# Kernel tuning notes

Hardware: AMD Instinct MI355X
Metric: run time of the kernel (lower is better)

## Reference

```python
import jax, jax.numpy as jnp
import numpy as np


def setup_inputs() -> dict:
    key = jax.random.key(0)
    x = jax.random.normal(key, (32, 512, 56, 56), dtype=jnp.float32)
    return {"x": x}


def reference(x):
    n, c, h, w = x.shape
    f = x.reshape(n, c, h * w)                       # (n, c, hw)
    f_norm = jax.nn.softmax(f * 7.0, axis=2)         # softmax over spatial
    bilinear = jnp.einsum('ncs,nds->ncd', f_norm, f) # (n, c, c)
    bilinear = jax.nn.softmax(bilinear, axis=2)      # softmax over channel 'keys'
    trilinear = jnp.einsum('ncd,nds->ncs', bilinear, f).reshape(n, c, h, w)
    trilinear = jax.lax.stop_gradient(trilinear)     # matches torch .detach()
    structure_att = jnp.sum(trilinear, axis=1, keepdims=True)  # (n, 1, h, w)
    return structure_att
```

## Files before the change

kernel.cpp:

```cpp
#include <hip/hip_runtime.h>
#include <stdint.h>


#define NB 32
#define CC 512
#define SS 3136
#define SCALE 7.0f
#define K7F 10.098865286222744f
#define INVK7F 0.09902102579427789f

typedef float f32x4 __attribute__((ext_vector_type(4)));
typedef _Float16 f16x8 __attribute__((ext_vector_type(8)));
typedef _Float16 f16x4 __attribute__((ext_vector_type(4)));
typedef _Float16 f16x2 __attribute__((ext_vector_type(2)));

__device__ inline unsigned short f2bf(float f) {
  unsigned int u = __float_as_uint(f);
  u += 0x7fffu + ((u >> 16) & 1u);
  return (unsigned short)(u >> 16);
}
__device__ inline float bf2f(unsigned short u) {
  return __uint_as_float((uint32_t)u << 16);
}

__device__ inline float fast_exp2(float v) {
  float r;
  asm("v_exp_f32 %0, %1" : "=v"(r) : "v"(v));
  return r;
}
__device__ inline uint32_t pk2h(float a, float b) {
  uint32_t r;
  asm("v_cvt_pkrtz_f16_f32 %0, %1, %2" : "=v"(r) : "v"(a), "v"(b));
  return r;
}
__device__ inline f16x8 exp2_f16x8(f16x8 h) {
  f16x8 r;
#pragma unroll
  for (int q = 0; q < 4; q++) {
    const float e0 = fast_exp2((float)h[2 * q]);
    const float e1 = fast_exp2((float)h[2 * q + 1]);
    ((uint32_t*)&r)[q] = pk2h(e0, e1);
  }
  return r;
}

__device__ inline float wredmax(float v) {
#pragma unroll
  for (int m = 32; m >= 1; m >>= 1) v = fmaxf(v, __shfl_xor(v, m, 64));
  return v;
}
__device__ inline float wredsum(float v) {
#pragma unroll
  for (int m = 32; m >= 1; m >>= 1) v += __shfl_xor(v, m, 64);
  return v;
}

__device__ inline void load_lds16(const void* g, void* l) {
  __builtin_amdgcn_global_load_lds(
      (const __attribute__((address_space(1))) void*)(uintptr_t)g,
      (__attribute__((address_space(3))) void*)(uintptr_t)l, 16, 0, 0);
}

__global__ __launch_bounds__(256) void k_prep(const float* __restrict__ x,
                                              unsigned short* __restrict__ t,
                                              float* __restrict__ inv7,
                                              float* __restrict__ mxv,
                                              float* __restrict__ esum) {
  const int row = blockIdx.x;
  const int tid = threadIdx.x;
  if (tid == 0) esum[row] = 0.f;
  const float4* xr = (const float4*)(x + (size_t)row * SS);
  float4 v0 = xr[tid];
  float4 v1 = xr[tid + 256];
  float4 v2 = xr[tid + 512];
  float4 v3 = (tid < 16) ? xr[768 + tid] : make_float4(-1e30f, -1e30f, -1e30f, -1e30f);

  float mx = fmaxf(fmaxf(fmaxf(v0.x, v0.y), fmaxf(v0.z, v0.w)),
             fmaxf(fmaxf(fmaxf(v1.x, v1.y), fmaxf(v1.z, v1.w)),
             fmaxf(fmaxf(fmaxf(v2.x, v2.y), fmaxf(v2.z, v2.w)),
                   fmaxf(fmaxf(v3.x, v3.y), fmaxf(v3.z, v3.w)))));
  __shared__ float redm[4], reds[4];
  mx = wredmax(mx);
  if ((tid & 63) == 0) redm[tid >> 6] = mx;
  __syncthreads();
  mx = fmaxf(fmaxf(redm[0], redm[1]), fmaxf(redm[2], redm[3]));

  float s = 0.f;
  f16x4 p0, p1, p2, p3;
#define TQ2(dst, i0, a0, a1)                                  \
  {                                                           \
    _Float16 h0 = (_Float16)(K7F * ((a0) - mx));              \
    _Float16 h1 = (_Float16)(K7F * ((a1) - mx));              \
    dst[i0] = h0; dst[i0 + 1] = h1;                           \
    uint32_t u = pk2h(fast_exp2((float)h0), fast_exp2((float)h1)); \
    f16x2 e2; *(uint32_t*)&e2 = u;                            \
    s += (float)e2[0] + (float)e2[1];                         \
  }
  TQ2(p0, 0, v0.x, v0.y) TQ2(p0, 2, v0.z, v0.w)
  TQ2(p1, 0, v1.x, v1.y) TQ2(p1, 2, v1.z, v1.w)
  TQ2(p2, 0, v2.x, v2.y) TQ2(p2, 2, v2.z, v2.w)
  TQ2(p3, 0, v3.x, v3.y) TQ2(p3, 2, v3.z, v3.w)
#undef TQ2
  s = wredsum(s);
  if ((tid & 63) == 0) reds[tid >> 6] = s;
  __syncthreads();

  f16x4* tr = (f16x4*)(t + (size_t)row * SS);
  tr[tid] = p0;
  tr[tid + 256] = p1;
  tr[tid + 512] = p2;
  if (tid < 16) tr[768 + tid] = p3;
  if (tid == 0) {
    const float stot = reds[0] + reds[1] + reds[2] + reds[3];
    inv7[row] = 1.0f / (K7F * stot);
    mxv[row] = mx;
  }
}

#define BM 128
#define BK 64
#define NT (SS / BK)

__global__ __launch_bounds__(256, 2) void k_gemm(const unsigned short* __restrict__ T,
                                                 unsigned short* __restrict__ P,
                                                 const float* __restrict__ inv7,
                                                 const float* __restrict__ mxv,
                                                 float* __restrict__ esum) {
  __shared__ unsigned short sA[2][BM * BK];
  __shared__ unsigned short sB[2][BM * BK];
  const int lin  = blockIdx.y * gridDim.x + blockIdx.x;
  const int xcd  = lin & 7;
  const int slot = lin >> 3;
  const int pair = xcd * 16 + (slot >> 2);
  const int n    = pair >> 2;
  const int tm   = (pair & 3) * BM;
  const int tn   = (slot & 3) * BM;
  const unsigned short* Ap = T + (size_t)n * CC * SS + (size_t)tm * SS;
  const unsigned short* Bp = T + (size_t)n * CC * SS + (size_t)tn * SS;
  const int tid  = threadIdx.x;
  const int lane = tid & 63;
  const int wave = tid >> 6;
  const int wm   = (wave >> 1) * 64;
  const int wn   = (wave & 1) * 64;
  const int quad = lane >> 4;
  const int rr   = lane & 15;

  int jb[4];
  const unsigned short *Aaddr[4], *Baddr[4];
#pragma unroll
  for (int tt = 0; tt < 4; tt++) {
    const int j  = ((tt << 2) + wave) * 64 + lane;
    const int r  = j >> 3;
    const int cg = (j & 7) ^ (r & 7);
    jb[tt]   = j * 8;
    Aaddr[tt] = Ap + (size_t)r * SS + cg * 8;
    Baddr[tt] = Bp + (size_t)r * SS + cg * 8;
  }

  f32x4 acc[4][4] = {};

#define COMPUTE(BUF)                                                          \
  {                                                                           \
    _Pragma("unroll")                                                         \
    for (int ki = 0; ki < 2; ki++) {                                          \
      f16x8 af[4], bfr[4];                                                    \
      const int cg = ki * 4 + quad;                                           \
      _Pragma("unroll")                                                       \
      for (int mt = 0; mt < 4; mt++) {                                        \
        const int r  = wm + mt * 16 + rr;                                     \
        const int cs = cg ^ (r & 7);                                          \
        af[mt] = *(const f16x8*)&sA[BUF][(r * 8 + cs) * 8];                   \
      }                                                                       \
      _Pragma("unroll")                                                       \
      for (int nt = 0; nt < 4; nt++) {                                        \
        const int r  = wn + nt * 16 + rr;                                     \
        const int cs = cg ^ (r & 7);                                          \
        bfr[nt] = *(const f16x8*)&sB[BUF][(r * 8 + cs) * 8];                  \
      }                                                                       \
      _Pragma("unroll")                                                       \
      for (int mt = 0; mt < 4; mt++)                                          \
        _Pragma("unroll")                                                     \
        for (int nt = 0; nt < 4; nt++)                                        \
          acc[mt][nt] = __builtin_amdgcn_mfma_f32_16x16x32_f16(               \
              af[mt], bfr[nt], acc[mt][nt], 0, 0, 0);                         \
    }                                                                         \
  }

  {
    f16x8 hv[4];
#pragma unroll
    for (int tt = 0; tt < 4; tt++) hv[tt] = *(const f16x8*)Aaddr[tt];
#pragma unroll
    for (int tt = 0; tt < 4; tt++) load_lds16(Baddr[tt], &sB[0][jb[tt]]);
#pragma unroll
    for (int tt = 0; tt < 4; tt++) *(f16x8*)&sA[0][jb[tt]] = exp2_f16x8(hv[tt]);
    __syncthreads();
  }

  int cur = 0;
  for (int t = 0; t < NT - 1; t++) {
    const int koff = (t + 1) * BK;
    const int nxt  = cur ^ 1;
    f16x8 hvN[4];
#pragma unroll
    for (int tt = 0; tt < 4; tt++) hvN[tt] = *(const f16x8*)(Aaddr[tt] + koff);
#pragma unroll
    for (int tt = 0; tt < 4; tt++) load_lds16(Baddr[tt] + koff, &sB[nxt][jb[tt]]);

    COMPUTE(cur);

#pragma unroll
    for (int tt = 0; tt < 4; tt++) *(f16x8*)&sA[nxt][jb[tt]] = exp2_f16x8(hvN[tt]);
    __syncthreads();
    cur = nxt;
  }
  COMPUTE(cur);

  unsigned short* Pp = P + ((size_t)n << 18);
  float mxd[4];
#pragma unroll
  for (int nt = 0; nt < 4; nt++) mxd[nt] = mxv[n * CC + tn + wn + nt * 16 + rr];
#pragma unroll
  for (int mt = 0; mt < 4; mt++) {
    const int rbase = tm + wm + mt * 16 + quad * 4;
    float iv[4];
#pragma unroll
    for (int i = 0; i < 4; i++) iv[i] = inv7[n * CC + rbase + i];
    float rs[4] = {0.f, 0.f, 0.f, 0.f};
#pragma unroll
    for (int nt = 0; nt < 4; nt++) {
      const int col = tn + wn + nt * 16 + rr;
#pragma unroll
      for (int i = 0; i < 4; i++) {
        const float e = __expf(acc[mt][nt][i] * iv[i] + mxd[nt]);
        rs[i] += e;
        Pp[(size_t)(rbase + i) * CC + col] = f2bf(e);
      }
    }
#pragma unroll
    for (int i = 0; i < 4; i++) {
      float v = rs[i];
#pragma unroll
      for (int m = 8; m >= 1; m >>= 1) v += __shfl_xor(v, m, 64);
      if (rr == 0) atomicAdd(&esum[n * CC + rbase + i], v);
    }
  }
#undef COMPUTE
}

__global__ __launch_bounds__(256) void k_wsum(const unsigned short* __restrict__ P,
                                              const float* __restrict__ esum,
                                              float* __restrict__ wp,
                                              float* __restrict__ outz) {
  const int lin  = blockIdx.y * gridDim.x + blockIdx.x;
  const int xcd  = lin & 7;
  const int slot = lin >> 3;
  const int n    = xcd * 4 + (slot & 3);
  const int g    = (slot >> 2) & 7;
  const int d    = (slot >> 5) * 256 + threadIdx.x;
  __shared__ float sinv[64];
  if (threadIdx.x < 64) sinv[threadIdx.x] = 1.0f / esum[n * CC + g * 64 + threadIdx.x];
  __syncthreads();
  const unsigned short* p = P + (size_t)n * CC * CC + (size_t)(g * 64) * CC + d;
  float acc = 0.f;
#pragma unroll 8
  for (int c = 0; c < 64; c++) acc += bf2f(p[(size_t)c * CC]) * sinv[c];
  wp[((size_t)n * 8 + g) * CC + d] = acc;
  const int idx = lin * 256 + threadIdx.x;
  if (idx < NB * SS) outz[idx] = 0.f;
}

__global__ __launch_bounds__(256) void k_out(const unsigned short* __restrict__ T,
                                             const float* __restrict__ wp,
                                             const float* __restrict__ mxv,
                                             float* __restrict__ out) {
  const int n  = blockIdx.y >> 2;
  const int dq = blockIdx.y & 3;
  const int s0 = (blockIdx.x * 256 + threadIdx.x) * 2;
  __shared__ float sw[128];
  __shared__ float sc[2];
  if (threadIdx.x < 128) {
    float v = 0.f;
#pragma unroll
    for (int g = 0; g < 8; g++) v += wp[((size_t)n * 8 + g) * CC + dq * 128 + threadIdx.x];
    sw[threadIdx.x] = v * INVK7F;
    float pm = v * mxv[n * CC + dq * 128 + threadIdx.x];
    pm = wredsum(pm);
    if ((threadIdx.x & 63) == 0) sc[threadIdx.x >> 6] = pm;
  }
  __syncthreads();
  const float csum = sc[0] + sc[1];
  if (s0 >= SS) return;
  const unsigned short* bp = T + (size_t)n * CC * SS + (size_t)(dq * 128) * SS + s0;
  float a0 = 0.f, a1 = 0.f;
#pragma unroll 8
  for (int d = 0; d < 128; d++) {
    const f16x2 hv = *(const f16x2*)(bp + (size_t)d * SS);
    a0 += sw[d] * (float)hv[0];
    a1 += sw[d] * (float)hv[1];
  }
  atomicAdd(&out[(size_t)n * SS + s0], a0 + csum);
  atomicAdd(&out[(size_t)n * SS + s0 + 1], a1 + csum);
}

extern "C" void kernel_launch(void* const* d_in, const int* in_sizes, int n_in,
                              void* d_out, int out_size, void* d_ws, size_t ws_size,
                              hipStream_t stream) {
  const float* x = (const float*)d_in[0];
  float* out = (float*)d_out;
  char* ws = (char*)d_ws;
  unsigned short* t    = (unsigned short*)ws;
  unsigned short* pmat = (unsigned short*)(ws + 102760448ull);
  float* esum = (float*)(ws + 119537664ull);
  float* inv7 = (float*)(ws + 119603200ull);
  float* mxv  = (float*)(ws + 119668736ull);
  float* wp   = (float*)(ws + 119734272ull);

  hipLaunchKernelGGL(k_prep, dim3(NB * CC),   dim3(256), 0, stream, x, t, inv7, mxv, esum);
  hipLaunchKernelGGL(k_gemm, dim3(16, NB),    dim3(256), 0, stream, t, pmat, inv7, mxv, esum);
  hipLaunchKernelGGL(k_wsum, dim3(16, NB),    dim3(256), 0, stream, pmat, esum, wp, out);
  hipLaunchKernelGGL(k_out,  dim3(7, NB * 4), dim3(256), 0, stream, t, wp, mxv, out);
}
```

Measured before the change: 145.9 us.

## Use 8-wave GEMM blocks and drop atomics in output reduction kernel

The GEMM kernel now runs 512 threads (8 waves) per 128x128 tile, with each wave owning a 64x32 sub-tile and loading half as many global chunks. This halves per-thread accumulators and raises waves per CU to hide latency, at the cost of more LDS reads per MFMA for the A fragments. Separately, the output kernel now has each block reduce over all 512 channels instead of a quarter, so it writes results directly rather than with atomicAdd. That also removes the need to zero the output inside the weighted-sum kernel, but leaves fewer blocks (224) for the output pass.

Result: slower. 154.1 us (+5.6%).

```diff
diff --git a/kernel.cpp b/kernel.cpp
--- a/kernel.cpp
+++ b/kernel.cpp
@@ -121,7 +121,7 @@
 #define BK 64
 #define NT (SS / BK)
 
-__global__ __launch_bounds__(256, 2) void k_gemm(const unsigned short* __restrict__ T,
+__global__ __launch_bounds__(512, 4) void k_gemm(const unsigned short* __restrict__ T,
                                                  unsigned short* __restrict__ P,
                                                  const float* __restrict__ inv7,
                                                  const float* __restrict__ mxv,
@@ -140,16 +140,16 @@
   const int tid  = threadIdx.x;
   const int lane = tid & 63;
   const int wave = tid >> 6;
-  const int wm   = (wave >> 1) * 64;
-  const int wn   = (wave & 1) * 64;
+  const int wm   = (wave >> 2) * 64;
+  const int wn   = (wave & 3) * 32;
   const int quad = lane >> 4;
   const int rr   = lane & 15;
 
-  int jb[4];
-  const unsigned short *Aaddr[4], *Baddr[4];
-#pragma unroll
-  for (int tt = 0; tt < 4; tt++) {
-    const int j  = ((tt << 2) + wave) * 64 + lane;
+  int jb[2];
+  const unsigned short *Aaddr[2], *Baddr[2];
+#pragma unroll
+  for (int tt = 0; tt < 2; tt++) {
+    const int j  = ((tt << 3) + wave) * 64 + lane;
     const int r  = j >> 3;
     const int cg = (j & 7) ^ (r & 7);
     jb[tt]   = j * 8;
@@ -157,13 +157,13 @@
     Baddr[tt] = Bp + (size_t)r * SS + cg * 8;
   }
 
-  f32x4 acc[4][4] = {};
+  f32x4 acc[4][2] = {};
 
 #define COMPUTE(BUF)                                                          \
   {                                                                           \
     _Pragma("unroll")                                                         \
     for (int ki = 0; ki < 2; ki++) {                                          \
-      f16x8 af[4], bfr[4];                                                    \
+      f16x8 af[4], bfr[2];                                                    \
       const int cg = ki * 4 + quad;                                           \
       _Pragma("unroll")                                                       \
       for (int mt = 0; mt < 4; mt++) {                                        \
@@ -172,7 +172,7 @@
         af[mt] = *(const f16x8*)&sA[BUF][(r * 8 + cs) * 8];                   \
       }                                                                       \
       _Pragma("unroll")                                                       \
-      for (int nt = 0; nt < 4; nt++) {                                        \
+      for (int nt = 0; nt < 2; nt++) {                                        \
         const int r  = wn + nt * 16 + rr;                                     \
         const int cs = cg ^ (r & 7);                                          \
         bfr[nt] = *(const f16x8*)&sB[BUF][(r * 8 + cs) * 8];                  \
@@ -180,20 +180,20 @@
       _Pragma("unroll")                                                       \
       for (int mt = 0; mt < 4; mt++)                                          \
         _Pragma("unroll")                                                     \
-        for (int nt = 0; nt < 4; nt++)                                        \
+        for (int nt = 0; nt < 2; nt++)                                        \
           acc[mt][nt] = __builtin_amdgcn_mfma_f32_16x16x32_f16(               \
               af[mt], bfr[nt], acc[mt][nt], 0, 0, 0);                         \
     }                                                                         \
   }
 
   {
-    f16x8 hv[4];
-#pragma unroll
-    for (int tt = 0; tt < 4; tt++) hv[tt] = *(const f16x8*)Aaddr[tt];
-#pragma unroll
-    for (int tt = 0; tt < 4; tt++) load_lds16(Baddr[tt], &sB[0][jb[tt]]);
-#pragma unroll
-    for (int tt = 0; tt < 4; tt++) *(f16x8*)&sA[0][jb[tt]] = exp2_f16x8(hv[tt]);
+    f16x8 hv[2];
+#pragma unroll
+    for (int tt = 0; tt < 2; tt++) hv[tt] = *(const f16x8*)Aaddr[tt];
+#pragma unroll
+    for (int tt = 0; tt < 2; tt++) load_lds16(Baddr[tt], &sB[0][jb[tt]]);
+#pragma unroll
+    for (int tt = 0; tt < 2; tt++) *(f16x8*)&sA[0][jb[tt]] = exp2_f16x8(hv[tt]);
     __syncthreads();
   }
 
@@ -201,25 +201,25 @@
   for (int t = 0; t < NT - 1; t++) {
     const int koff = (t + 1) * BK;
     const int nxt  = cur ^ 1;
-    f16x8 hvN[4];
-#pragma unroll
-    for (int tt = 0; tt < 4; tt++) hvN[tt] = *(const f16x8*)(Aaddr[tt] + koff);
-#pragma unroll
-    for (int tt = 0; tt < 4; tt++) load_lds16(Baddr[tt] + koff, &sB[nxt][jb[tt]]);
+    f16x8 hvN[2];
+#pragma unroll
+    for (int tt = 0; tt < 2; tt++) hvN[tt] = *(const f16x8*)(Aaddr[tt] + koff);
+#pragma unroll
+    for (int tt = 0; tt < 2; tt++) load_lds16(Baddr[tt] + koff, &sB[nxt][jb[tt]]);
 
     COMPUTE(cur);
 
 #pragma unroll
-    for (int tt = 0; tt < 4; tt++) *(f16x8*)&sA[nxt][jb[tt]] = exp2_f16x8(hvN[tt]);
+    for (int tt = 0; tt < 2; tt++) *(f16x8*)&sA[nxt][jb[tt]] = exp2_f16x8(hvN[tt]);
     __syncthreads();
     cur = nxt;
   }
   COMPUTE(cur);
 
   unsigned short* Pp = P + ((size_t)n << 18);
-  float mxd[4];
-#pragma unroll
-  for (int nt = 0; nt < 4; nt++) mxd[nt] = mxv[n * CC + tn + wn + nt * 16 + rr];
+  float mxd[2];
+#pragma unroll
+  for (int nt = 0; nt < 2; nt++) mxd[nt] = mxv[n * CC + tn + wn + nt * 16 + rr];
 #pragma unroll
   for (int mt = 0; mt < 4; mt++) {
     const int rbase = tm + wm + mt * 16 + quad * 4;
@@ -228,7 +228,7 @@
     for (int i = 0; i < 4; i++) iv[i] = inv7[n * CC + rbase + i];
     float rs[4] = {0.f, 0.f, 0.f, 0.f};
 #pragma unroll
-    for (int nt = 0; nt < 4; nt++) {
+    for (int nt = 0; nt < 2; nt++) {
       const int col = tn + wn + nt * 16 + rr;
 #pragma unroll
       for (int i = 0; i < 4; i++) {
@@ -250,8 +250,7 @@
 
 __global__ __launch_bounds__(256) void k_wsum(const unsigned short* __restrict__ P,
                                               const float* __restrict__ esum,
-                                              float* __restrict__ wp,
-                                              float* __restrict__ outz) {
+                                              float* __restrict__ wp) {
   const int lin  = blockIdx.y * gridDim.x + blockIdx.x;
   const int xcd  = lin & 7;
   const int slot = lin >> 3;
@@ -266,41 +265,40 @@
 #pragma unroll 8
   for (int c = 0; c < 64; c++) acc += bf2f(p[(size_t)c * CC]) * sinv[c];
   wp[((size_t)n * 8 + g) * CC + d] = acc;
-  const int idx = lin * 256 + threadIdx.x;
-  if (idx < NB * SS) outz[idx] = 0.f;
 }
 
 __global__ __launch_bounds__(256) void k_out(const unsigned short* __restrict__ T,
                                              const float* __restrict__ wp,
                                              const float* __restrict__ mxv,
                                              float* __restrict__ out) {
-  const int n  = blockIdx.y >> 2;
-  const int dq = blockIdx.y & 3;
+  const int n  = blockIdx.y;
   const int s0 = (blockIdx.x * 256 + threadIdx.x) * 2;
-  __shared__ float sw[128];
-  __shared__ float sc[2];
-  if (threadIdx.x < 128) {
+  __shared__ float sw[512];
+  __shared__ float sc[4];
+  float pm = 0.f;
+#pragma unroll
+  for (int dd = threadIdx.x; dd < 512; dd += 256) {
     float v = 0.f;
 #pragma unroll
-    for (int g = 0; g < 8; g++) v += wp[((size_t)n * 8 + g) * CC + dq * 128 + threadIdx.x];
-    sw[threadIdx.x] = v * INVK7F;
-    float pm = v * mxv[n * CC + dq * 128 + threadIdx.x];
-    pm = wredsum(pm);
-    if ((threadIdx.x & 63) == 0) sc[threadIdx.x >> 6] = pm;
-  }
+    for (int g = 0; g < 8; g++) v += wp[((size_t)n * 8 + g) * CC + dd];
+    sw[dd] = v * INVK7F;
+    pm += v * mxv[n * CC + dd];
+  }
+  pm = wredsum(pm);
+  if ((threadIdx.x & 63) == 0) sc[threadIdx.x >> 6] = pm;
   __syncthreads();
-  const float csum = sc[0] + sc[1];
+  const float csum = sc[0] + sc[1] + sc[2] + sc[3];
   if (s0 >= SS) return;
-  const unsigned short* bp = T + (size_t)n * CC * SS + (size_t)(dq * 128) * SS + s0;
+  const unsigned short* bp = T + (size_t)n * CC * SS + s0;
   float a0 = 0.f, a1 = 0.f;
 #pragma unroll 8
-  for (int d = 0; d < 128; d++) {
+  for (int d = 0; d < 512; d++) {
     const f16x2 hv = *(const f16x2*)(bp + (size_t)d * SS);
     a0 += sw[d] * (float)hv[0];
     a1 += sw[d] * (float)hv[1];
   }
-  atomicAdd(&out[(size_t)n * SS + s0], a0 + csum);
-  atomicAdd(&out[(size_t)n * SS + s0 + 1], a1 + csum);
+  out[(size_t)n * SS + s0]     = a0 + csum;
+  out[(size_t)n * SS + s0 + 1] = a1 + csum;
 }
 
 extern "C" void kernel_launch(void* const* d_in, const int* in_sizes, int n_in,
@@ -317,7 +315,7 @@
   float* wp   = (float*)(ws + 119734272ull);
 
   hipLaunchKernelGGL(k_prep, dim3(NB * CC),   dim3(256), 0, stream, x, t, inv7, mxv, esum);
-  hipLaunchKernelGGL(k_gemm, dim3(16, NB),    dim3(256), 0, stream, t, pmat, inv7, mxv, esum);
-  hipLaunchKernelGGL(k_wsum, dim3(16, NB),    dim3(256), 0, stream, pmat, esum, wp, out);
-  hipLaunchKernelGGL(k_out,  dim3(7, NB * 4), dim3(256), 0, stream, t, wp, mxv, out);
-}
+  hipLaunchKernelGGL(k_gemm, dim3(16, NB),    dim3(512), 0, stream, t, pmat, inv7, mxv, esum);
+  hipLaunchKernelGGL(k_wsum, dim3(16, NB),    dim3(256), 0, stream, pmat, esum, wp);
+  hipLaunchKernelGGL(k_out,  dim3(7, NB),     dim3(256), 0, stream, t, wp, mxv, out);
+}
```

## Load GEMM B operand directly from global into registers, drop LDS staging

Applied to the files above, without the earlier changes.

Removes the shared-memory buffer for the B tile: each wave now reads its B fragments straight from global memory into registers inside the compute step, instead of staging them through LDS with global_load_lds. This halves the LDS footprint, and the launch bound is raised to allow three blocks per CU. The trade-off is that B loads are no longer prefetched a tile ahead, so global latency sits on the MFMA critical path. Each B row is also read by both wave pairs sharing it, which adds redundant global/L2 traffic.

Result: slower. 189.8 us (+30.0%).

```diff
diff --git a/kernel.cpp b/kernel.cpp
--- a/kernel.cpp
+++ b/kernel.cpp
@@ -53,12 +53,6 @@
 #pragma unroll
   for (int m = 32; m >= 1; m >>= 1) v += __shfl_xor(v, m, 64);
   return v;
-}
-
-__device__ inline void load_lds16(const void* g, void* l) {
-  __builtin_amdgcn_global_load_lds(
-      (const __attribute__((address_space(1))) void*)(uintptr_t)g,
-      (__attribute__((address_space(3))) void*)(uintptr_t)l, 16, 0, 0);
 }
 
 __global__ __launch_bounds__(256) void k_prep(const float* __restrict__ x,
@@ -121,13 +115,12 @@
 #define BK 64
 #define NT (SS / BK)
 
-__global__ __launch_bounds__(256, 2) void k_gemm(const unsigned short* __restrict__ T,
+__global__ __launch_bounds__(256, 3) void k_gemm(const unsigned short* __restrict__ T,
                                                  unsigned short* __restrict__ P,
                                                  const float* __restrict__ inv7,
                                                  const float* __restrict__ mxv,
                                                  float* __restrict__ esum) {
   __shared__ unsigned short sA[2][BM * BK];
-  __shared__ unsigned short sB[2][BM * BK];
   const int lin  = blockIdx.y * gridDim.x + blockIdx.x;
   const int xcd  = lin & 7;
   const int slot = lin >> 3;
@@ -146,7 +139,7 @@
   const int rr   = lane & 15;
 
   int jb[4];
-  const unsigned short *Aaddr[4], *Baddr[4];
+  const unsigned short* Aaddr[4];
 #pragma unroll
   for (int tt = 0; tt < 4; tt++) {
     const int j  = ((tt << 2) + wave) * 64 + lane;
@@ -154,16 +147,24 @@
     const int cg = (j & 7) ^ (r & 7);
     jb[tt]   = j * 8;
     Aaddr[tt] = Ap + (size_t)r * SS + cg * 8;
-    Baddr[tt] = Bp + (size_t)r * SS + cg * 8;
-  }
+  }
+  const unsigned short* Brow[4];
+#pragma unroll
+  for (int nt = 0; nt < 4; nt++)
+    Brow[nt] = Bp + (size_t)(wn + nt * 16 + rr) * SS + quad * 8;
 
   f32x4 acc[4][4] = {};
 
-#define COMPUTE(BUF)                                                          \
+#define COMPUTE(BUF, K0)                                                      \
   {                                                                           \
+    f16x8 bg0[4], bg1[4];                                                     \
+    _Pragma("unroll")                                                         \
+    for (int nt = 0; nt < 4; nt++) bg0[nt] = *(const f16x8*)(Brow[nt] + (K0));\
+    _Pragma("unroll")                                                         \
+    for (int nt = 0; nt < 4; nt++) bg1[nt] = *(const f16x8*)(Brow[nt] + (K0) + 32);\
     _Pragma("unroll")                                                         \
     for (int ki = 0; ki < 2; ki++) {                                          \
-      f16x8 af[4], bfr[4];                                                    \
+      f16x8 af[4];                                                            \
       const int cg = ki * 4 + quad;                                           \
       _Pragma("unroll")                                                       \
       for (int mt = 0; mt < 4; mt++) {                                        \
@@ -172,17 +173,11 @@
         af[mt] = *(const f16x8*)&sA[BUF][(r * 8 + cs) * 8];                   \
       }                                                                       \
       _Pragma("unroll")                                                       \
-      for (int nt = 0; nt < 4; nt++) {                                        \
-        const int r  = wn + nt * 16 + rr;                                     \
-        const int cs = cg ^ (r & 7);                                          \
-        bfr[nt] = *(const f16x8*)&sB[BUF][(r * 8 + cs) * 8];                  \
-      }                                                                       \
-      _Pragma("unroll")                                                       \
       for (int mt = 0; mt < 4; mt++)                                          \
         _Pragma("unroll")                                                     \
         for (int nt = 0; nt < 4; nt++)                                        \
           acc[mt][nt] = __builtin_amdgcn_mfma_f32_16x16x32_f16(               \
-              af[mt], bfr[nt], acc[mt][nt], 0, 0, 0);                         \
+              af[mt], (ki ? bg1[nt] : bg0[nt]), acc[mt][nt], 0, 0, 0);        \
     }                                                                         \
   }
 
@@ -191,30 +186,26 @@
 #pragma unroll
     for (int tt = 0; tt < 4; tt++) hv[tt] = *(const f16x8*)Aaddr[tt];
 #pragma unroll
-    for (int tt = 0; tt < 4; tt++) load_lds16(Baddr[tt], &sB[0][jb[tt]]);
-#pragma unroll
     for (int tt = 0; tt < 4; tt++) *(f16x8*)&sA[0][jb[tt]] = exp2_f16x8(hv[tt]);
     __syncthreads();
   }
 
   int cur = 0;
   for (int t = 0; t < NT - 1; t++) {
-    const int koff = (t + 1) * BK;
+    const int k0   = t * BK;
     const int nxt  = cur ^ 1;
     f16x8 hvN[4];
 #pragma unroll
-    for (int tt = 0; tt < 4; tt++) hvN[tt] = *(const f16x8*)(Aaddr[tt] + koff);
-#pragma unroll
-    for (int tt = 0; tt < 4; tt++) load_lds16(Baddr[tt] + koff, &sB[nxt][jb[tt]]);
-
-    COMPUTE(cur);
+    for (int tt = 0; tt < 4; tt++) hvN[tt] = *(const f16x8*)(Aaddr[tt] + k0 + BK);
+
+    COMPUTE(cur, k0);
 
 #pragma unroll
     for (int tt = 0; tt < 4; tt++) *(f16x8*)&sA[nxt][jb[tt]] = exp2_f16x8(hvN[tt]);
     __syncthreads();
     cur = nxt;
   }
-  COMPUTE(cur);
+  COMPUTE(cur, (NT - 1) * BK);
 
   unsigned short* Pp = P + ((size_t)n << 18);
   float mxd[4];
```

## Triple-buffer B tiles and prefetch two K-steps ahead in GEMM

Applied to the files above, without the earlier changes.

The shared-memory B tile becomes a three-slot ring, and both the LDS-direct B loads and the register loads of A are issued two K-steps ahead instead of one. The main loop is unrolled by two so the A register buffers alternate between iterations. The full __syncthreads is replaced with an explicit lgkmcnt wait plus s_barrier. The aim is to hide more global-memory latency behind the MFMA work. In exchange it uses more LDS and holds more live registers, which could hurt occupancy at two blocks per CU.

Result: no change. 147.7 us (+1.2%).

```diff
diff --git a/kernel.cpp b/kernel.cpp
--- a/kernel.cpp
+++ b/kernel.cpp
@@ -59,6 +59,12 @@
   __builtin_amdgcn_global_load_lds(
       (const __attribute__((address_space(1))) void*)(uintptr_t)g,
       (__attribute__((address_space(3))) void*)(uintptr_t)l, 16, 0, 0);
+}
+
+__device__ inline void barrier_lgkm() {
+  asm volatile("s_waitcnt lgkmcnt(0)" ::: "memory");
+  __builtin_amdgcn_s_barrier();
+  asm volatile("" ::: "memory");
 }
 
 __global__ __launch_bounds__(256) void k_prep(const float* __restrict__ x,
@@ -120,14 +126,15 @@
 #define BM 128
 #define BK 64
 #define NT (SS / BK)
+#define TBUF (BM * BK)
 
 __global__ __launch_bounds__(256, 2) void k_gemm(const unsigned short* __restrict__ T,
                                                  unsigned short* __restrict__ P,
                                                  const float* __restrict__ inv7,
                                                  const float* __restrict__ mxv,
                                                  float* __restrict__ esum) {
-  __shared__ unsigned short sA[2][BM * BK];
-  __shared__ unsigned short sB[2][BM * BK];
+  __shared__ unsigned short sA[2 * TBUF];
+  __shared__ unsigned short sB[3 * TBUF];
   const int lin  = blockIdx.y * gridDim.x + blockIdx.x;
   const int xcd  = lin & 7;
   const int slot = lin >> 3;
@@ -159,7 +166,7 @@
 
   f32x4 acc[4][4] = {};
 
-#define COMPUTE(BUF)                                                          \
+#define COMPUTE(SBO, SAO)                                                     \
   {                                                                           \
     _Pragma("unroll")                                                         \
     for (int ki = 0; ki < 2; ki++) {                                          \
@@ -169,13 +176,13 @@
       for (int mt = 0; mt < 4; mt++) {                                        \
         const int r  = wm + mt * 16 + rr;                                     \
         const int cs = cg ^ (r & 7);                                          \
-        af[mt] = *(const f16x8*)&sA[BUF][(r * 8 + cs) * 8];                   \
+        af[mt] = *(const f16x8*)&sA[(SAO) + (r * 8 + cs) * 8];                \
       }                                                                       \
       _Pragma("unroll")                                                       \
       for (int nt = 0; nt < 4; nt++) {                                        \
         const int r  = wn + nt * 16 + rr;                                     \
         const int cs = cg ^ (r & 7);                                          \
-        bfr[nt] = *(const f16x8*)&sB[BUF][(r * 8 + cs) * 8];                  \
+        bfr[nt] = *(const f16x8*)&sB[(SBO) + (r * 8 + cs) * 8];               \
       }                                                                       \
       _Pragma("unroll")                                                       \
       for (int mt = 0; mt < 4; mt++)                                          \
@@ -186,35 +193,49 @@
     }                                                                         \
   }
 
+  f16x8 hvA[4], hvB[4];
+
   {
-    f16x8 hv[4];
-#pragma unroll
-    for (int tt = 0; tt < 4; tt++) hv[tt] = *(const f16x8*)Aaddr[tt];
-#pragma unroll
-    for (int tt = 0; tt < 4; tt++) load_lds16(Baddr[tt], &sB[0][jb[tt]]);
-#pragma unroll
-    for (int tt = 0; tt < 4; tt++) *(f16x8*)&sA[0][jb[tt]] = exp2_f16x8(hv[tt]);
-    __syncthreads();
-  }
-
-  int cur = 0;
-  for (int t = 0; t < NT - 1; t++) {
-    const int koff = (t + 1) * BK;
-    const int nxt  = cur ^ 1;
-    f16x8 hvN[4];
-#pragma unroll
-    for (int tt = 0; tt < 4; tt++) hvN[tt] = *(const f16x8*)(Aaddr[tt] + koff);
-#pragma unroll
-    for (int tt = 0; tt < 4; tt++) load_lds16(Baddr[tt] + koff, &sB[nxt][jb[tt]]);
-
-    COMPUTE(cur);
-
-#pragma unroll
-    for (int tt = 0; tt < 4; tt++) *(f16x8*)&sA[nxt][jb[tt]] = exp2_f16x8(hvN[tt]);
-    __syncthreads();
-    cur = nxt;
-  }
-  COMPUTE(cur);
+#pragma unroll
+    for (int tt = 0; tt < 4; tt++) load_lds16(Baddr[tt], &sB[jb[tt]]);
+#pragma unroll
+    for (int tt = 0; tt < 4; tt++) load_lds16(Baddr[tt] + BK, &sB[TBUF + jb[tt]]);
+#pragma unroll
+    for (int tt = 0; tt < 4; tt++) hvA[tt] = *(const f16x8*)Aaddr[tt];
+#pragma unroll
+    for (int tt = 0; tt < 4; tt++) hvB[tt] = *(const f16x8*)(Aaddr[tt] + BK);
+#pragma unroll
+    for (int tt = 0; tt < 4; tt++) *(f16x8*)&sA[jb[tt]] = exp2_f16x8(hvA[tt]);
+    barrier_lgkm();
+  }
+
+  int sbR = 0, sbN = TBUF, sbW = 2 * TBUF;
+  int aR = 0, aW = TBUF;
+
+#define BODY(T, HVU, HVF)                                                     \
+  {                                                                           \
+    if ((T) + 2 < NT) {                                                       \
+      const int ko = ((T) + 2) * BK;                                          \
+      _Pragma("unroll")                                                       \
+      for (int tt = 0; tt < 4; tt++) load_lds16(Baddr[tt] + ko, &sB[sbW + jb[tt]]); \
+      _Pragma("unroll")                                                       \
+      for (int tt = 0; tt < 4; tt++) HVF[tt] = *(const f16x8*)(Aaddr[tt] + ko); \
+    }                                                                         \
+    COMPUTE(sbR, aR);                                                         \
+    if ((T) + 1 < NT) {                                                       \
+      _Pragma("unroll")                                                       \
+      for (int tt = 0; tt < 4; tt++) *(f16x8*)&sA[aW + jb[tt]] = exp2_f16x8(HVU[tt]); \
+      barrier_lgkm();                                                         \
+    }                                                                         \
+    const int o = sbR; sbR = sbN; sbN = sbW; sbW = o;                         \
+    const int a = aR; aR = aW; aW = a;                                        \
+  }
+
+  for (int t = 0; t < NT; t += 2) {
+    BODY(t, hvB, hvA);
+    if (t + 1 < NT) BODY(t + 1, hvA, hvB);
+  }
+#undef BODY
 
   unsigned short* Pp = P + ((size_t)n << 18);
   float mxd[4];
```
